# Kernel tuning notes

Measured on AMD Instinct MI355X. Metric: run time of the kernel, lower is better.

The kernel has to match this reference:

```python
import jax, jax.numpy as jnp
import numpy as np

N = 50000
E = 1600000
EPS = 1e-16


def transformer_conv(x, src, dst, ea, Wq, bq, Wk, bk, Wv, bv, We, Ws, bs):
    # PyG TransformerConv, heads=1, concat=True, root_weight=True
    C = Wq.shape[1]
    q = x @ Wq + bq                      # [N, C]
    k = x @ Wk + bk                      # [N, C]
    v = x @ Wv + bv                      # [N, C]
    e = ea @ We                          # [E, C]
    k_e = k[src] + e                     # per-edge key
    v_e = v[src] + e                     # per-edge value
    score = (q[dst] * k_e).sum(-1) / jnp.sqrt(jnp.asarray(C, x.dtype))  # [E]
    # segment softmax over incoming edges of each dst node
    m = jax.ops.segment_max(score, dst, num_segments=N)
    ex = jnp.exp(score - m[dst])
    denom = jax.ops.segment_sum(ex, dst, num_segments=N)
    alpha = ex / (denom[dst] + EPS)
    out = jax.ops.segment_sum(alpha[:, None] * v_e, dst, num_segments=N)
    return out + x @ Ws + bs             # skip connection


def gcn_conv(x, src, dst, W, b):
    # PyG GCNConv: self-loops + symmetric deg^-1/2 normalization
    n_idx = jnp.arange(N)
    src2 = jnp.concatenate([src, n_idx])
    dst2 = jnp.concatenate([dst, n_idx])
    deg = jax.ops.segment_sum(jnp.ones(E + N, x.dtype), dst2, num_segments=N)
    dinv = jnp.where(deg > 0, jax.lax.rsqrt(deg), 0.0)
    norm = dinv[src2] * dinv[dst2]       # [E+N]
    h = x @ W                            # [N, out]
    out = jax.ops.segment_sum(norm[:, None] * h[src2], dst2, num_segments=N)
    return out + b


def setup_inputs() -> dict:
    key = jax.random.key(0)
    ks = jax.random.split(key, 32)
    d = {}
    d['x'] = jax.random.normal(ks[0], (N, 128), jnp.float32)
    d['edge_index'] = jax.random.randint(ks[1], (2, E), 0, N, jnp.int64)
    d['edge_attr'] = jax.random.normal(ks[2], (E, 16), jnp.float32)
    shapes = dict(
        Wq1=(128, 96), bq1=(96,), Wk1=(128, 96), bk1=(96,), Wv1=(128, 96), bv1=(96,),
        We1=(16, 96), Ws1=(128, 96), bs1=(96,),
        Wq2=(96, 64), bq2=(64,), Wk2=(96, 64), bk2=(64,), Wv2=(96, 64), bv2=(64,),
        We2=(16, 64), Ws2=(96, 64), bs2=(64,),
        Wmu=(64, 32), bmu=(32,), Wls=(64, 32), bls=(32,))
    for i, (name, shp) in enumerate(shapes.items()):
        scale = 1.0 / np.sqrt(shp[0]) if len(shp) == 2 else 0.02
        d[name] = jax.random.normal(ks[3 + i], shp, jnp.float32) * scale
    return d


def reference(x, edge_index, edge_attr,
              Wq1, bq1, Wk1, bk1, Wv1, bv1, We1, Ws1, bs1,
              Wq2, bq2, Wk2, bk2, Wv2, bv2, We2, Ws2, bs2,
              Wmu, bmu, Wls, bls):
    src, dst = edge_index[0], edge_index[1]
    h = jax.nn.relu(transformer_conv(x, src, dst, edge_attr,
                                     Wq1, bq1, Wk1, bk1, Wv1, bv1, We1, Ws1, bs1))
    h = jax.nn.relu(transformer_conv(h, src, dst, edge_attr,
                                     Wq2, bq2, Wk2, bk2, Wv2, bv2, We2, Ws2, bs2))
    mu = gcn_conv(h, src, dst, Wmu, bmu)
    logstd = gcn_conv(h, src, dst, Wls, bls)
    return mu, logstd
```

## Files before the change

kernel.cpp:

```cpp
#include <hip/hip_runtime.h>
#include <math.h>


#define TPB 256
typedef unsigned int uint32;
typedef unsigned long long u64;
typedef unsigned short u16;
typedef __attribute__((ext_vector_type(4))) float f32x4;
typedef __attribute__((ext_vector_type(4))) uint32 u32x4;
typedef __attribute__((ext_vector_type(4))) int i32x4;
typedef __attribute__((ext_vector_type(8))) short bf16x8;

__device__ __forceinline__ uint32 f2bf(float f) {
    uint32 u = __float_as_uint(f);
    return (u + 0x7fffu + ((u >> 16) & 1u)) >> 16;
}
__device__ __forceinline__ float bf2f(uint32 b) { return __uint_as_float(b << 16); }

__global__ void hist_kernel(const int* __restrict__ dst, int* __restrict__ deg, int E) {
    int base = (blockIdx.x * TPB + threadIdx.x) * 8;
    if (base + 8 <= E) {
        i32x4 d0 = __builtin_nontemporal_load((const i32x4*)(dst + base));
        i32x4 d1 = __builtin_nontemporal_load((const i32x4*)(dst + base + 4));
        atomicAdd(&deg[d0.x], 1); atomicAdd(&deg[d0.y], 1);
        atomicAdd(&deg[d0.z], 1); atomicAdd(&deg[d0.w], 1);
        atomicAdd(&deg[d1.x], 1); atomicAdd(&deg[d1.y], 1);
        atomicAdd(&deg[d1.z], 1); atomicAdd(&deg[d1.w], 1);
    } else {
        for (int i = base; i < E; ++i) atomicAdd(&deg[dst[i]], 1);
    }
}

__global__ __launch_bounds__(1024) void scan1_kernel(const int* __restrict__ deg,
                                                     int* __restrict__ prowp,
                                                     int* __restrict__ bsum, int n) {
    __shared__ int wsum[16];
    __shared__ int woff[16];
    int tid = threadIdx.x;
    int i = blockIdx.x * 1024 + tid;
    int lane = tid & 63, w = tid >> 6;
    int dg = (i < n) ? deg[i] : 0;
    int x = (dg + 7) & ~7;
    int v = x;
#pragma unroll
    for (int off = 1; off < 64; off <<= 1) {
        int t = __shfl_up(v, off, 64);
        if (lane >= off) v += t;
    }
    if (lane == 63) wsum[w] = v;
    __syncthreads();
    if (tid < 64) {
        int s = (tid < 16) ? wsum[tid] : 0;
#pragma unroll
        for (int off = 1; off < 16; off <<= 1) {
            int t = __shfl_up(s, off, 64);
            if (lane >= off) s += t;
        }
        if (tid < 16) woff[tid] = s;
    }
    __syncthreads();
    int incl = v + (w ? woff[w - 1] : 0);
    if (i < n) prowp[i] = incl;
    if (tid == 1023) bsum[blockIdx.x] = incl;
}

__global__ void scan2_kernel(const int* __restrict__ bsum, int* __restrict__ boff,
                             int* __restrict__ prowpN, int nb) {
    int tid = threadIdx.x;
    int x = (tid < nb) ? bsum[tid] : 0;
    int v = x;
#pragma unroll
    for (int off = 1; off < 64; off <<= 1) {
        int t = __shfl_up(v, off, 64);
        if (tid >= off) v += t;
    }
    if (tid < nb) boff[tid] = v - x;
    if (tid == nb - 1) *prowpN = v;
}

__global__ __launch_bounds__(1024) void scan3_kernel(const int* __restrict__ deg,
                                                     const int* __restrict__ boff,
                                                     int* __restrict__ prowp,
                                                     int* __restrict__ cursor,
                                                     float* __restrict__ dinv,
                                                     u64* __restrict__ pse, int n) {
    int i = blockIdx.x * 1024 + threadIdx.x;
    if (i < n) {
        int dg = deg[i];
        int x = (dg + 7) & ~7;
        int excl = prowp[i] - x + boff[blockIdx.x];
        prowp[i] = excl;
        cursor[i] = excl;
        dinv[i] = 1.0f / sqrtf((float)(dg + 1));
        u64 pad = (u64)(uint32)n;
        for (int p = excl + dg; p < excl + x; ++p) pse[p] = pad;
    }
}

__global__ void scatter_kernel(const int* __restrict__ src, const int* __restrict__ dst,
                               int* __restrict__ cursor, u64* __restrict__ pse, int E) {
    int base = (blockIdx.x * TPB + threadIdx.x) * 8;
    if (base + 8 <= E) {
        i32x4 s0 = __builtin_nontemporal_load((const i32x4*)(src + base));
        i32x4 s1 = __builtin_nontemporal_load((const i32x4*)(src + base + 4));
        i32x4 d0 = __builtin_nontemporal_load((const i32x4*)(dst + base));
        i32x4 d1 = __builtin_nontemporal_load((const i32x4*)(dst + base + 4));
        int sv[8] = {s0.x, s0.y, s0.z, s0.w, s1.x, s1.y, s1.z, s1.w};
        int dv[8] = {d0.x, d0.y, d0.z, d0.w, d1.x, d1.y, d1.z, d1.w};
        int pos[8];
#pragma unroll
        for (int u = 0; u < 8; ++u) pos[u] = atomicAdd(&cursor[dv[u]], 1);
#pragma unroll
        for (int u = 0; u < 8; ++u)
            pse[pos[u]] = ((u64)(uint32)(base + u) << 32) | (uint32)sv[u];
    } else {
        for (int i = base; i < E; ++i) {
            int pos = atomicAdd(&cursor[dst[i]], 1);
            pse[pos] = ((u64)(uint32)i << 32) | (uint32)src[i];
        }
    }
}

__global__ void permute_kernel(const u64* __restrict__ pse, const float* __restrict__ EA,
                               const int* __restrict__ prowpN,
                               int* __restrict__ psrc, u16* __restrict__ EAb,
                               int N, int cap) {
    int i = blockIdx.x * TPB + threadIdx.x;
    if (i >= cap) return;
    int tot = *prowpN;
    if (i >= tot) return;
    u64 pk = __builtin_nontemporal_load(pse + i);
    uint32 s = (uint32)pk;
    uint32 eid = (uint32)(pk >> 32);
    __builtin_nontemporal_store((int)s, psrc + i);
    u32x4 lo = {0u, 0u, 0u, 0u}, hi = {0u, 0u, 0u, 0u};
    if (s != (uint32)N) {
        const f32x4* e4 = (const f32x4*)(EA + (size_t)eid * 16);
        f32x4 a = __builtin_nontemporal_load(e4);
        f32x4 b = __builtin_nontemporal_load(e4 + 1);
        f32x4 c = __builtin_nontemporal_load(e4 + 2);
        f32x4 d = __builtin_nontemporal_load(e4 + 3);
        lo = (u32x4){f2bf(a.x) | (f2bf(a.y) << 16), f2bf(a.z) | (f2bf(a.w) << 16),
                     f2bf(b.x) | (f2bf(b.y) << 16), f2bf(b.z) | (f2bf(b.w) << 16)};
        hi = (u32x4){f2bf(c.x) | (f2bf(c.y) << 16), f2bf(c.z) | (f2bf(c.w) << 16),
                     f2bf(d.x) | (f2bf(d.y) << 16), f2bf(d.z) | (f2bf(d.w) << 16)};
    }
    u32x4* o = (u32x4*)(EAb + (size_t)i * 16);
    __builtin_nontemporal_store(lo, o);
    __builtin_nontemporal_store(hi, o + 1);
}

__global__ void pack_kernel(
    const float* Wq1, const float* Wk1, const float* Wv1, const float* Ws1,
    const float* bq1, const float* bk1, const float* bv1, const float* bs1,
    const float* We1,
    const float* Wq2, const float* Wk2, const float* Wv2, const float* Ws2,
    const float* bq2, const float* bk2, const float* bv2, const float* bs2,
    const float* We2,
    const float* Wmu, const float* bmu, const float* Wls, const float* bls,
    const float* x, unsigned short* xb, int NX,
    unsigned short* Wc1t, float* bc1, unsigned short* Wc2t, float* bc2,
    float* Wc3, float* bc3) {
    const float s1 = 0.1020620726159658f;
    const float s2 = 0.125f;
    int gi = blockIdx.x * TPB + threadIdx.x;
    const int R0 = 448 * 128, R1 = R0 + 320 * 96, R2 = R1 + 64 * 64;
    const int R3 = R2 + 448, R4 = R3 + 320, R5 = R4 + 64;
    for (int i = gi; i < R5; i += gridDim.x * TPB) {
        if (i < R0) {
            int c = i / 128, kk = i % 128;
            float v = 0.f;
            if (c < 96) v = Wq1[kk * 96 + c] * s1;
            else if (c < 112) {
                int t = c - 96; float a = 0.f;
                for (int u = 0; u < 96; ++u) a += Wq1[kk * 96 + u] * We1[t * 96 + u];
                v = a * s1;
            } else if (c < 304) {
                int tt = c - 112;
                v = (tt & 1) ? Wv1[kk * 96 + (tt >> 1)] : Wk1[kk * 96 + (tt >> 1)];
            } else if (c < 400) v = Ws1[kk * 96 + (c - 304)];
            Wc1t[i] = (unsigned short)f2bf(v);
        } else if (i < R1) {
            int j = i - R0;
            int c = j / 96, kk = j % 96;
            float v = 0.f;
            if (c < 64) v = Wq2[kk * 64 + c] * s2;
            else if (c < 80) {
                int t = c - 64; float a = 0.f;
                for (int u = 0; u < 64; ++u) a += Wq2[kk * 64 + u] * We2[t * 64 + u];
                v = a * s2;
            } else if (c < 208) {
                int tt = c - 80;
                v = (tt & 1) ? Wv2[kk * 64 + (tt >> 1)] : Wk2[kk * 64 + (tt >> 1)];
            } else if (c < 272) v = Ws2[kk * 64 + (c - 208)];
            Wc2t[j] = (unsigned short)f2bf(v);
        } else if (i < R2) {
            int j = i - R1;
            int k = j / 64, c = j % 64;
            Wc3[j] = (c < 32) ? Wmu[k * 32 + c] : Wls[k * 32 + (c - 32)];
        } else if (i < R3) {
            int c = i - R2;
            float v = 0.f;
            if (c < 96) v = bq1[c] * s1;
            else if (c < 112) {
                int t = c - 96; float a = 0.f;
                for (int u = 0; u < 96; ++u) a += bq1[u] * We1[t * 96 + u];
                v = a * s1;
            } else if (c < 304) {
                int tt = c - 112;
                v = (tt & 1) ? bv1[tt >> 1] : bk1[tt >> 1];
            } else if (c < 400) v = bs1[c - 304];
            bc1[c] = v;
        } else if (i < R4) {
            int c = i - R3;
            float v = 0.f;
            if (c < 64) v = bq2[c] * s2;
            else if (c < 80) {
                int t = c - 64; float a = 0.f;
                for (int u = 0; u < 64; ++u) a += bq2[u] * We2[t * 64 + u];
                v = a * s2;
            } else if (c < 208) {
                int tt = c - 80;
                v = (tt & 1) ? bv2[tt >> 1] : bk2[tt >> 1];
            } else if (c < 272) v = bs2[c - 208];
            bc2[c] = v;
        } else {
            int c = i - R4;
            bc3[c] = (c < 32) ? bmu[c] : bls[c - 32];
        }
    }
    for (int i = gi; i < NX; i += gridDim.x * TPB)
        xb[i] = (unsigned short)f2bf(x[i]);
}

__global__ __launch_bounds__(256) void mfma_gemm_kernel(
    const unsigned short* __restrict__ A,
    const unsigned short* __restrict__ Wt,
    const float* __restrict__ bias,
    float* __restrict__ Qs, float* __restrict__ QE,
    uint32* __restrict__ KVp, float* __restrict__ SK,
    int N, int K, int Cq) {
    __shared__ unsigned short As[64][56];
    __shared__ unsigned short Bs[64][56];
    int r0 = blockIdx.x * 64, c0 = blockIdx.y * 64;
    int tid = threadIdx.x;
    int lane = tid & 63, w = tid >> 6;
    int wm = w >> 1, wn = w & 1;
    int l15 = lane & 15, l4 = lane >> 4;
    f32x4 zero = {0.f, 0.f, 0.f, 0.f};
    f32x4 acc[2][2] = {{zero, zero}, {zero, zero}};
    int sr = tid >> 2, sk = (tid & 3) * 8;

    for (int kc = 0; kc < K; kc += 32) {
        bf16x8 av = {};
        int ar = r0 + sr;
        if (ar < N) av = *(const bf16x8*)(A + (size_t)ar * K + kc + sk);
        *(bf16x8*)&As[sr][sk] = av;
        bf16x8 bv = *(const bf16x8*)(Wt + (size_t)(c0 + sr) * K + kc + sk);
        *(bf16x8*)&Bs[sr][sk] = bv;
        __syncthreads();
        bf16x8 af0 = *(const bf16x8*)&As[32 * wm + l15][l4 * 8];
        bf16x8 af1 = *(const bf16x8*)&As[32 * wm + 16 + l15][l4 * 8];
        bf16x8 bf0 = *(const bf16x8*)&Bs[32 * wn + l15][l4 * 8];
        bf16x8 bf1 = *(const bf16x8*)&Bs[32 * wn + 16 + l15][l4 * 8];
        acc[0][0] = __builtin_amdgcn_mfma_f32_16x16x32_bf16(af0, bf0, acc[0][0], 0, 0, 0);
        acc[0][1] = __builtin_amdgcn_mfma_f32_16x16x32_bf16(af0, bf1, acc[0][1], 0, 0, 0);
        acc[1][0] = __builtin_amdgcn_mfma_f32_16x16x32_bf16(af1, bf0, acc[1][0], 0, 0, 0);
        acc[1][1] = __builtin_amdgcn_mfma_f32_16x16x32_bf16(af1, bf1, acc[1][1], 0, 0, 0);
        __syncthreads();
    }

    int qe0 = Cq, kv0 = Cq + 16, sk0 = 3 * Cq + 16, end0 = 4 * Cq + 16;
#pragma unroll
    for (int fm = 0; fm < 2; ++fm) {
#pragma unroll
        for (int fn = 0; fn < 2; ++fn) {
            int cb = c0 + 32 * wn + 16 * fn;
            int c = cb + l15;
            float bia = bias[c];
#pragma unroll
            for (int r = 0; r < 4; ++r) {
                int row = r0 + 32 * wm + 16 * fm + l4 * 4 + r;
                float v = acc[fm][fn][r] + bia;
                float pv = __shfl_xor(v, 1, 64);
                bool ok = row < N;
                if (cb < qe0) {
                    if (ok) Qs[(size_t)row * Cq + c] = v;
                } else if (cb < kv0) {
                    if (ok) QE[(size_t)row * 16 + (c - qe0)] = v;
                } else if (cb < sk0) {
                    if (ok && !(l15 & 1)) {
                        int t = c - kv0;
                        KVp[(size_t)row * Cq + (t >> 1)] = (f2bf(v) << 16) | f2bf(pv);
                    }
                } else if (cb < end0) {
                    if (ok) SK[(size_t)row * Cq + (c - sk0)] = v;
                }
            }
        }
    }
}

template <int C>
__global__ __launch_bounds__(256) void edge_attn_kernel(
    const float* __restrict__ Qs, const float* __restrict__ SK,
    const uint32* __restrict__ KVp,
    const u16* __restrict__ EAb, const float* __restrict__ QE,
    const int* __restrict__ prowp, const int* __restrict__ deg,
    const int* __restrict__ psrc,
    float* __restrict__ Hpre, float* __restrict__ AEA, int N) {
    constexpr int CPL = C / 32;
    int n = blockIdx.x * 4 + (threadIdx.x >> 6);
    if (n >= N) return;
    int lane = threadIdx.x & 63;
    int half = lane >> 5, l = lane & 31, t16 = l & 15;
    bool lo16 = (l < 16);

    uint32 nC = (uint32)n * C;
    float q[CPL], acc[CPL];
#pragma unroll
    for (int j = 0; j < CPL; ++j) { q[j] = Qs[nC + l + 32 * j]; acc[j] = 0.f; }
    float qe = lo16 ? QE[(uint32)n * 16 + t16] : 0.f;
    float d = 0.f, aea = 0.f;
    int eb = prowp[n], ee = prowp[n + 1];

    for (int base = eb + 8 * half; base < ee; base += 16) {
        const int* sp = psrc + base;
        const u16* ep = EAb + (size_t)base * 16 + t16;
        float dots[8], eav[8];
        uint32 kv[8][CPL];
#pragma unroll
        for (int u = 0; u < 8; ++u) {
            int s = __builtin_nontemporal_load(sp + u);
            eav[u] = bf2f(__builtin_nontemporal_load(ep + u * 16));
            uint32 off = (uint32)s * C + l;
            float dt = qe * eav[u];
#pragma unroll
            for (int j = 0; j < CPL; ++j) {
                uint32 t = KVp[off + 32 * j];
                kv[u][j] = t;
                dt = fmaf(q[j], __uint_as_float(t & 0xffff0000u), dt);
            }
            dots[u] = dt;
        }
#pragma unroll
        for (int a = 0; a < 4; ++a) {
            float x0 = dots[2 * a], x1 = dots[2 * a + 1];
            float z = (lo16 ? x0 : x1) + __shfl_xor(lo16 ? x1 : x0, 16, 64);
            z += __shfl_xor(z, 8, 64);
            z += __shfl_xor(z, 4, 64);
            z += __shfl_xor(z, 2, 64);
            z += __shfl_xor(z, 1, 64);
            float p = __expf(z);
            float p0 = __shfl(p, 0, 32);
            float p1 = __shfl(p, 16, 32);
            d += p0 + p1;
            aea = fmaf(p0, eav[2 * a], fmaf(p1, eav[2 * a + 1], aea));
#pragma unroll
            for (int j = 0; j < CPL; ++j)
                acc[j] = fmaf(p0, __uint_as_float(kv[2 * a][j] << 16),
                         fmaf(p1, __uint_as_float(kv[2 * a + 1][j] << 16), acc[j]));
        }
    }
    d += __shfl_xor(d, 32, 64);
    aea += __shfl_xor(aea, 32, 64);
    d -= (float)((ee - eb) - deg[n]);
    float inv = 1.f / (d + 1e-16f);
#pragma unroll
    for (int j = 0; j < CPL; ++j) {
        float a2 = acc[j] + __shfl_xor(acc[j], 32, 64);
        if (half == 0)
            Hpre[nC + l + 32 * j] = a2 * inv + SK[nC + l + 32 * j];
    }
    if (lane < 16) AEA[(uint32)n * 16 + t16] = aea * inv;
}

template <int C>
__global__ void fixup_relu_kernel(const float* __restrict__ Hpre, const float* __restrict__ AEA,
                                  const float* __restrict__ We,
                                  unsigned short* __restrict__ H1b, int NC) {
    int idx = blockIdx.x * TPB + threadIdx.x;
    if (idx >= NC) return;
    int n = idx / C, c = idx % C;
    const float* a = AEA + (size_t)n * 16;
    float s = Hpre[idx];
#pragma unroll
    for (int t = 0; t < 16; ++t) s += a[t] * We[t * C + c];
    H1b[idx] = (unsigned short)f2bf(fmaxf(s, 0.f));
}

__global__ void fixup2_kernel(const float* __restrict__ Hpre, const float* __restrict__ AEA,
                              const float* __restrict__ We, const float* __restrict__ dinv,
                              uint32* __restrict__ H2p, int N) {
    int idx = blockIdx.x * TPB + threadIdx.x;
    if (idx >= N * 32) return;
    int n = idx >> 5, c = idx & 31;
    const float* a = AEA + (size_t)n * 16;
    float s0 = Hpre[(size_t)n * 64 + c];
    float s1 = Hpre[(size_t)n * 64 + 32 + c];
#pragma unroll
    for (int t = 0; t < 16; ++t) {
        s0 += a[t] * We[t * 64 + c];
        s1 += a[t] * We[t * 64 + 32 + c];
    }
    float dn = dinv[n];
    s0 = fmaxf(s0, 0.f) * dn;
    s1 = fmaxf(s1, 0.f) * dn;
    H2p[idx] = f2bf(s0) | (f2bf(s1) << 16);
}

__global__ __launch_bounds__(256) void gcn_agg_kernel(
    const uint32* __restrict__ H2p, const int* __restrict__ prowp,
    const int* __restrict__ psrc, const float* __restrict__ dinv,
    float* __restrict__ AGG, int N) {
    int n = blockIdx.x * 4 + (threadIdx.x >> 6);
    if (n >= N) return;
    int lane = threadIdx.x & 63, half = lane >> 5, l = lane & 31;
    float s0 = 0.f, s1 = 0.f;
    int eb = prowp[n], ee = prowp[n + 1];
    for (int base = eb + 8 * half; base < ee; base += 16) {
        const int* sp = psrc + base;
#pragma unroll
        for (int u = 0; u < 8; ++u) {
            uint32 s = (uint32)__builtin_nontemporal_load(sp + u);
            uint32 t = H2p[s * 32 + l];
            s0 += bf2f(t & 0xffffu);
            s1 += __uint_as_float(t & 0xffff0000u);
        }
    }
    s0 += __shfl_xor(s0, 32, 64);
    s1 += __shfl_xor(s1, 32, 64);
    if (half == 0) {
        uint32 u = H2p[(uint32)n * 32 + l];
        float dn = dinv[n];
        AGG[(uint32)n * 64 + l]      = dn * (s0 + bf2f(u & 0xffffu));
        AGG[(uint32)n * 64 + 32 + l] = dn * (s1 + __uint_as_float(u & 0xffff0000u));
    }
}

template <int CT, bool SPLIT>
__global__ __launch_bounds__(256) void gemm_kernel(
    const float* __restrict__ A, const float* __restrict__ W,
    const float* __restrict__ bias, float* __restrict__ Out,
    float* __restrict__ Out2, int N, int K, int C) {
    constexpr int TC = CT / 16;
    __shared__ float As[32][68];
    __shared__ float Bs[32][CT + 4];
    int r0 = blockIdx.x * 64, c0 = blockIdx.y * CT;
    int t = threadIdx.x;
    int tr = t >> 4, tc = t & 15;
    float acc[4][TC];
#pragma unroll
    for (int i = 0; i < 4; ++i)
#pragma unroll
        for (int j = 0; j < TC; ++j) acc[i][j] = 0.f;

    for (int kc = 0; kc < K; kc += 32) {
        int ra = t >> 2, kq = (t & 3) * 8;
        float4 a0 = {0, 0, 0, 0}, a1 = {0, 0, 0, 0};
        int r = r0 + ra;
        if (r < N) {
            const float* ap = A + (size_t)r * K + kc + kq;
            a0 = *(const float4*)ap;
            a1 = *(const float4*)(ap + 4);
        }
        As[kq + 0][ra] = a0.x; As[kq + 1][ra] = a0.y;
        As[kq + 2][ra] = a0.z; As[kq + 3][ra] = a0.w;
        As[kq + 4][ra] = a1.x; As[kq + 5][ra] = a1.y;
        As[kq + 6][ra] = a1.z; As[kq + 7][ra] = a1.w;
        constexpr int PASSES = (32 * CT) / (256 * 8);
#pragma unroll
        for (int p = 0; p < PASSES; ++p) {
            int idx = (t + p * 256) * 8;
            int k = idx / CT, c = idx % CT;
            const float* wp = W + (size_t)(kc + k) * C + c0 + c;
            float4 b0 = *(const float4*)wp;
            float4 b1 = *(const float4*)(wp + 4);
            *(float4*)&Bs[k][c] = b0;
            *(float4*)&Bs[k][c + 4] = b1;
        }
        __syncthreads();
#pragma unroll
        for (int k = 0; k < 32; ++k) {
            float4 av = *(const float4*)&As[k][tr * 4];
            float a[4] = {av.x, av.y, av.z, av.w};
#pragma unroll
            for (int u = 0; u < TC / 4; ++u) {
                float4 bv = *(const float4*)&Bs[k][tc * TC + u * 4];
                float b[4] = {bv.x, bv.y, bv.z, bv.w};
#pragma unroll
                for (int i = 0; i < 4; ++i)
#pragma unroll
                    for (int j = 0; j < 4; ++j) acc[i][u * 4 + j] += a[i] * b[j];
            }
        }
        __syncthreads();
    }
#pragma unroll
    for (int i = 0; i < 4; ++i) {
        int r = r0 + tr * 4 + i;
        if (r >= N) continue;
#pragma unroll
        for (int j = 0; j < TC; ++j) {
            int c = c0 + tc * TC + j;
            float v = acc[i][j] + bias[c];
            if (SPLIT) {
                if (c < 32) Out[(size_t)r * 32 + c] = v;
                else        Out2[(size_t)r * 32 + c - 32] = v;
            } else {
                Out[(size_t)r * C + c] = v;
            }
        }
    }
}

extern "C" void kernel_launch(void* const* d_in, const int* in_sizes, int n_in,
                              void* d_out, int out_size, void* d_ws, size_t ws_size,
                              hipStream_t stream) {
    const float* x   = (const float*)d_in[0];
    const int*   ei  = (const int*)d_in[1];
    const float* ea  = (const float*)d_in[2];
    const float* Wq1 = (const float*)d_in[3];  const float* bq1 = (const float*)d_in[4];
    const float* Wk1 = (const float*)d_in[5];  const float* bk1 = (const float*)d_in[6];
    const float* Wv1 = (const float*)d_in[7];  const float* bv1 = (const float*)d_in[8];
    const float* We1 = (const float*)d_in[9];
    const float* Ws1 = (const float*)d_in[10]; const float* bs1 = (const float*)d_in[11];
    const float* Wq2 = (const float*)d_in[12]; const float* bq2 = (const float*)d_in[13];
    const float* Wk2 = (const float*)d_in[14]; const float* bk2 = (const float*)d_in[15];
    const float* Wv2 = (const float*)d_in[16]; const float* bv2 = (const float*)d_in[17];
    const float* We2 = (const float*)d_in[18];
    const float* Ws2 = (const float*)d_in[19]; const float* bs2 = (const float*)d_in[20];
    const float* Wmu = (const float*)d_in[21]; const float* bmu = (const float*)d_in[22];
    const float* Wls = (const float*)d_in[23]; const float* bls = (const float*)d_in[24];

    int N = in_sizes[0] / 128;
    int E = in_sizes[1] / 2;
    const int* src = ei;
    const int* dst = ei + E;
    int E2max = E + 8 * N;

    char* ws = (char*)d_ws;
    size_t off = 0;
    auto alloc = [&](size_t bytes) -> char* {
        char* p = ws + off;
        off = (off + bytes + 255) & ~(size_t)255;
        return p;
    };
    int*      deg    = (int*)alloc((size_t)N * 4);
    int*      prowp  = (int*)alloc((size_t)(N + 1) * 4);
    int*      cursor = (int*)alloc((size_t)N * 4);
    float*    dinv   = (float*)alloc((size_t)N * 4);
    int*      bsum   = (int*)alloc(256 * 4);
    int*      boff   = (int*)alloc(256 * 4);
    u64*      pse    = (u64*)alloc((size_t)E2max * 8);
    int*      psrc   = (int*)alloc((size_t)E2max * 4);
    u16*      EAb    = (u16*)alloc((size_t)E2max * 16 * 2);
    unsigned short* Wc1t = (unsigned short*)alloc(448 * 128 * 2);
    float*    bc1    = (float*)alloc(448 * 4);
    unsigned short* Wc2t = (unsigned short*)alloc(320 * 96 * 2);
    float*    bc2    = (float*)alloc(320 * 4);
    float*    Wc3    = (float*)alloc(64 * 64 * 4);
    float*    bc3    = (float*)alloc(64 * 4);
    unsigned short* xb = (unsigned short*)alloc((size_t)N * 128 * 2);
    float*    Qs   = (float*)alloc((size_t)N * 96 * 4);
    float*    QE   = (float*)alloc((size_t)N * 16 * 4);
    uint32*   KVp  = (uint32*)alloc((size_t)(N + 1) * 96 * 4);
    float*    SKb  = (float*)alloc((size_t)N * 96 * 4);
    float*    Hpre = (float*)alloc((size_t)N * 96 * 4);
    unsigned short* H1b = (unsigned short*)alloc((size_t)N * 96 * 2);
    float*    AEA  = (float*)alloc((size_t)N * 16 * 4);
    uint32*   H2p  = (uint32*)alloc((size_t)(N + 1) * 32 * 4);
    float*    AGG  = (float*)alloc((size_t)N * 64 * 4);

    (void)hipMemsetAsync(deg, 0, (size_t)N * 4, stream);
    (void)hipMemsetAsync(KVp + (size_t)N * 96, 0, 96 * 4, stream);
    (void)hipMemsetAsync(H2p + (size_t)N * 32, 0, 32 * 4, stream);

    int eb8 = (E + TPB * 8 - 1) / (TPB * 8);
    int e2bk = (E2max + TPB - 1) / TPB;
    int nb1k = (N + 1023) / 1024;
    hist_kernel<<<eb8, TPB, 0, stream>>>(dst, deg, E);
    scan1_kernel<<<nb1k, 1024, 0, stream>>>(deg, prowp, bsum, N);
    scan2_kernel<<<1, 64, 0, stream>>>(bsum, boff, prowp + N, nb1k);
    scan3_kernel<<<nb1k, 1024, 0, stream>>>(deg, boff, prowp, cursor, dinv, pse, N);
    scatter_kernel<<<eb8, TPB, 0, stream>>>(src, dst, cursor, pse, E);
    permute_kernel<<<e2bk, TPB, 0, stream>>>(pse, ea, prowp + N, psrc, EAb, N, E2max);
    pack_kernel<<<364, TPB, 0, stream>>>(Wq1, Wk1, Wv1, Ws1, bq1, bk1, bv1, bs1, We1,
                                         Wq2, Wk2, Wv2, Ws2, bq2, bk2, bv2, bs2, We2,
                                         Wmu, bmu, Wls, bls, x, xb, N * 128,
                                         Wc1t, bc1, Wc2t, bc2, Wc3, bc3);

    int rb = (N + 63) / 64;
    int nb4 = (N + 3) / 4;

    mfma_gemm_kernel<<<dim3(rb, 7), 256, 0, stream>>>(xb, Wc1t, bc1, Qs, QE, KVp, SKb,
                                                      N, 128, 96);
    edge_attn_kernel<96><<<nb4, 256, 0, stream>>>(Qs, SKb, KVp, EAb, QE, prowp, deg, psrc,
                                                  Hpre, AEA, N);
    fixup_relu_kernel<96><<<(N * 96 + TPB - 1) / TPB, TPB, 0, stream>>>(Hpre, AEA, We1,
                                                                        H1b, N * 96);
    mfma_gemm_kernel<<<dim3(rb, 5), 256, 0, stream>>>(H1b, Wc2t, bc2, Qs, QE, KVp, SKb,
                                                      N, 96, 64);
    (void)hipMemsetAsync(KVp + (size_t)N * 64, 0, 64 * 4, stream);
    edge_attn_kernel<64><<<nb4, 256, 0, stream>>>(Qs, SKb, KVp, EAb, QE, prowp, deg, psrc,
                                                  Hpre, AEA, N);
    fixup2_kernel<<<(N * 32 + TPB - 1) / TPB, TPB, 0, stream>>>(Hpre, AEA, We2, dinv, H2p, N);
    gcn_agg_kernel<<<nb4, 256, 0, stream>>>(H2p, prowp, psrc, dinv, AGG, N);
    gemm_kernel<64, true><<<dim3(rb, 1), 256, 0, stream>>>(AGG, Wc3, bc3, (float*)d_out,
                                                           (float*)d_out + (size_t)N * 32,
                                                           N, 64, 64);
}
```

Before: 616.1 us.

## Partition histogram and scatter atomics by destination range across block groups

The histogram and CSR scatter kernels now run as 8 block groups, each reading all edges but applying atomics only to destinations in its own node-range slice. Consecutive blocks belong to different groups. The intent is to concentrate atomic traffic on a smaller address range per group, improving L2 locality for the degree and cursor atomics and the pse writes. The cost is reading the src/dst arrays 8 times, and the fixed 2048-block grid-stride launch changes how work is spread.

```diff
diff --git a/kernel.cpp b/kernel.cpp
--- a/kernel.cpp
+++ b/kernel.cpp
@@ -3,6 +3,7 @@
 
 
 #define TPB 256
+#define NGRP 8
 typedef unsigned int uint32;
 typedef unsigned long long u64;
 typedef unsigned short u16;
@@ -17,17 +18,27 @@
 }
 __device__ __forceinline__ float bf2f(uint32 b) { return __uint_as_float(b << 16); }
 
-__global__ void hist_kernel(const int* __restrict__ dst, int* __restrict__ deg, int E) {
-    int base = (blockIdx.x * TPB + threadIdx.x) * 8;
-    if (base + 8 <= E) {
-        i32x4 d0 = __builtin_nontemporal_load((const i32x4*)(dst + base));
-        i32x4 d1 = __builtin_nontemporal_load((const i32x4*)(dst + base + 4));
-        atomicAdd(&deg[d0.x], 1); atomicAdd(&deg[d0.y], 1);
-        atomicAdd(&deg[d0.z], 1); atomicAdd(&deg[d0.w], 1);
-        atomicAdd(&deg[d1.x], 1); atomicAdd(&deg[d1.y], 1);
-        atomicAdd(&deg[d1.z], 1); atomicAdd(&deg[d1.w], 1);
-    } else {
-        for (int i = base; i < E; ++i) atomicAdd(&deg[dst[i]], 1);
+__global__ void hist_kernel(const int* __restrict__ dst, int* __restrict__ deg,
+                            int E, int span) {
+    int grp = blockIdx.x & (NGRP - 1);
+    int lo = grp * span;
+    int nb = gridDim.x >> 3;
+    int bid = blockIdx.x >> 3;
+    int stride = nb * TPB * 8;
+    for (int base = (bid * TPB + threadIdx.x) * 8; base < E; base += stride) {
+        if (base + 8 <= E) {
+            i32x4 d0 = __builtin_nontemporal_load((const i32x4*)(dst + base));
+            i32x4 d1 = __builtin_nontemporal_load((const i32x4*)(dst + base + 4));
+            int dv[8] = {d0.x, d0.y, d0.z, d0.w, d1.x, d1.y, d1.z, d1.w};
+#pragma unroll
+            for (int u = 0; u < 8; ++u)
+                if ((uint32)(dv[u] - lo) < (uint32)span) atomicAdd(&deg[dv[u]], 1);
+        } else {
+            for (int i = base; i < E; ++i) {
+                int d = dst[i];
+                if ((uint32)(d - lo) < (uint32)span) atomicAdd(&deg[d], 1);
+            }
+        }
     }
 }
 
@@ -98,25 +109,36 @@
 }
 
 __global__ void scatter_kernel(const int* __restrict__ src, const int* __restrict__ dst,
-                               int* __restrict__ cursor, u64* __restrict__ pse, int E) {
-    int base = (blockIdx.x * TPB + threadIdx.x) * 8;
-    if (base + 8 <= E) {
-        i32x4 s0 = __builtin_nontemporal_load((const i32x4*)(src + base));
-        i32x4 s1 = __builtin_nontemporal_load((const i32x4*)(src + base + 4));
-        i32x4 d0 = __builtin_nontemporal_load((const i32x4*)(dst + base));
-        i32x4 d1 = __builtin_nontemporal_load((const i32x4*)(dst + base + 4));
-        int sv[8] = {s0.x, s0.y, s0.z, s0.w, s1.x, s1.y, s1.z, s1.w};
-        int dv[8] = {d0.x, d0.y, d0.z, d0.w, d1.x, d1.y, d1.z, d1.w};
-        int pos[8];
-#pragma unroll
-        for (int u = 0; u < 8; ++u) pos[u] = atomicAdd(&cursor[dv[u]], 1);
-#pragma unroll
-        for (int u = 0; u < 8; ++u)
-            pse[pos[u]] = ((u64)(uint32)(base + u) << 32) | (uint32)sv[u];
-    } else {
-        for (int i = base; i < E; ++i) {
-            int pos = atomicAdd(&cursor[dst[i]], 1);
-            pse[pos] = ((u64)(uint32)i << 32) | (uint32)src[i];
+                               int* __restrict__ cursor, u64* __restrict__ pse,
+                               int E, int span) {
+    int grp = blockIdx.x & (NGRP - 1);
+    int lo = grp * span;
+    int nb = gridDim.x >> 3;
+    int bid = blockIdx.x >> 3;
+    int stride = nb * TPB * 8;
+    for (int base = (bid * TPB + threadIdx.x) * 8; base < E; base += stride) {
+        if (base + 8 <= E) {
+            i32x4 d0 = __builtin_nontemporal_load((const i32x4*)(dst + base));
+            i32x4 d1 = __builtin_nontemporal_load((const i32x4*)(dst + base + 4));
+            i32x4 s0 = __builtin_nontemporal_load((const i32x4*)(src + base));
+            i32x4 s1 = __builtin_nontemporal_load((const i32x4*)(src + base + 4));
+            int dv[8] = {d0.x, d0.y, d0.z, d0.w, d1.x, d1.y, d1.z, d1.w};
+            int sv[8] = {s0.x, s0.y, s0.z, s0.w, s1.x, s1.y, s1.z, s1.w};
+#pragma unroll
+            for (int u = 0; u < 8; ++u) {
+                if ((uint32)(dv[u] - lo) < (uint32)span) {
+                    int pos = atomicAdd(&cursor[dv[u]], 1);
+                    pse[pos] = ((u64)(uint32)(base + u) << 32) | (uint32)sv[u];
+                }
+            }
+        } else {
+            for (int i = base; i < E; ++i) {
+                int d = dst[i];
+                if ((uint32)(d - lo) < (uint32)span) {
+                    int pos = atomicAdd(&cursor[d], 1);
+                    pse[pos] = ((u64)(uint32)i << 32) | (uint32)src[i];
+                }
+            }
         }
     }
 }
@@ -538,6 +560,7 @@
     const int* src = ei;
     const int* dst = ei + E;
     int E2max = E + 8 * N;
+    int span = (N + NGRP - 1) / NGRP;
 
     char* ws = (char*)d_ws;
     size_t off = 0;
@@ -576,14 +599,13 @@
     (void)hipMemsetAsync(KVp + (size_t)N * 96, 0, 96 * 4, stream);
     (void)hipMemsetAsync(H2p + (size_t)N * 32, 0, 32 * 4, stream);
 
-    int eb8 = (E + TPB * 8 - 1) / (TPB * 8);
     int e2bk = (E2max + TPB - 1) / TPB;
     int nb1k = (N + 1023) / 1024;
-    hist_kernel<<<eb8, TPB, 0, stream>>>(dst, deg, E);
+    hist_kernel<<<2048, TPB, 0, stream>>>(dst, deg, E, span);
     scan1_kernel<<<nb1k, 1024, 0, stream>>>(deg, prowp, bsum, N);
     scan2_kernel<<<1, 64, 0, stream>>>(bsum, boff, prowp + N, nb1k);
     scan3_kernel<<<nb1k, 1024, 0, stream>>>(deg, boff, prowp, cursor, dinv, pse, N);
-    scatter_kernel<<<eb8, TPB, 0, stream>>>(src, dst, cursor, pse, E);
+    scatter_kernel<<<2048, TPB, 0, stream>>>(src, dst, cursor, pse, E, span);
     permute_kernel<<<e2bk, TPB, 0, stream>>>(pse, ea, prowp + N, psrc, EAb, N, E2max);
     pack_kernel<<<364, TPB, 0, stream>>>(Wq1, Wk1, Wv1, Ws1, bq1, bk1, bv1, bs1, We1,
                                          Wq2, Wk2, Wv2, Ws2, bq2, bk2, bv2, bs2, We2,
```

Result: faster. 567.6 us (-7.9%).
